# Optimization experiments

Measured on AMD Instinct MI355X. Metric: run time of the kernel, lower is better.

## Reference

```python
import jax, jax.numpy as jnp
import numpy as np

B, T, H, W, C = 2, 4, 128, 128, 192
HEADS = 6
WS = 8          # attention window (per-frame, wsD=1)
OW = 12         # overlapping KV window: 8 + int(8*0.5)
PAD = (OW - WS) // 2
TBL = (WS + OW - 1) ** 2   # 361 relative-position-bias entries
MLP_HID = C * 2


def setup_inputs() -> dict:
    key = jax.random.key(0)
    ks = jax.random.split(key, 8)
    s = 0.02
    return dict(
        x=jax.random.normal(ks[0], (B, T, H, W, C), jnp.float32),
        x_size=jnp.array([H, W], jnp.int32),  # unused by forward (shadowed), kept for signature fidelity
        rpi_oca=jax.random.randint(ks[1], (WS * WS, OW * OW), 0, TBL),
        norm1_g=jnp.ones((C,), jnp.float32), norm1_b=jnp.zeros((C,), jnp.float32),
        qkv_w=jax.random.normal(ks[2], (C, 3 * C), jnp.float32) * s,
        qkv_b=jnp.zeros((3 * C,), jnp.float32),
        rpb_table=jax.random.normal(ks[3], (TBL, HEADS), jnp.float32) * s,
        norm2_g=jnp.ones((C,), jnp.float32), norm2_b=jnp.zeros((C,), jnp.float32),
        fc1_w=jax.random.normal(ks[4], (C, MLP_HID), jnp.float32) * s,
        fc1_b=jnp.zeros((MLP_HID,), jnp.float32),
        fc2_w=jax.random.normal(ks[5], (MLP_HID, C), jnp.float32) * s,
        fc2_b=jnp.zeros((C,), jnp.float32),
    )


def _ln(x, g, b):
    m = x.mean(-1, keepdims=True)
    v = ((x - m) ** 2).mean(-1, keepdims=True)
    return (x - m) * jax.lax.rsqrt(v + 1e-5) * g + b


def reference(x, x_size, rpi_oca, norm1_g, norm1_b, qkv_w, qkv_b, rpb_table,
              norm2_g, norm2_b, fc1_w, fc1_b, fc2_w, fc2_b):
    b, t, h, w, c = x.shape
    d = c // HEADS
    scale = d ** -0.5
    nH, nW = h // WS, w // WS
    b_ = b * t * nH * nW  # total windows
    shortcut = x
    xn = _ln(x, norm1_g, norm1_b)
    qkv = (xn @ qkv_w + qkv_b).reshape(b, t, h, w, 3, c)
    q, k, v = qkv[..., 0, :], qkv[..., 1, :], qkv[..., 2, :]
    # --- query: non-overlapping (1,8,8) windows -> (b_, heads, 64, d)
    qw = (q.reshape(b, t, nH, WS, nW, WS, c)
           .transpose(0, 1, 2, 4, 3, 5, 6)
           .reshape(b_, WS * WS, HEADS, d)
           .transpose(0, 2, 1, 3))
    # --- key/value: overlapping (1,12,12) windows with stride 8, zero-padded by 2
    hid = (jnp.arange(nH) * WS)[:, None] + jnp.arange(OW)  # (nH, OW)
    wid = (jnp.arange(nW) * WS)[:, None] + jnp.arange(OW)  # (nW, OW)

    def owin(z):
        zp = jnp.pad(z, ((0, 0), (0, 0), (PAD, PAD), (PAD, PAD), (0, 0)))
        zw = zp[:, :, hid][:, :, :, :, wid]  # (b, t, nH, OW, nW, OW, c)
        return (zw.transpose(0, 1, 2, 4, 3, 5, 6)
                  .reshape(b_, OW * OW, HEADS, d)
                  .transpose(0, 2, 1, 3))

    kw, vw = owin(k), owin(v)
    attn = jnp.einsum('bhqd,bhkd->bhqk', qw * scale, kw)  # (b_, heads, 64, 144)
    bias = rpb_table[rpi_oca.reshape(-1)].reshape(WS * WS, OW * OW, HEADS).transpose(2, 0, 1)
    attn = attn + bias[None]  # NOTE: original forward applies NO softmax (self.softmax unused)
    out = (jnp.einsum('bhqk,bhkd->bhqd', attn, vw)
             .transpose(0, 2, 1, 3)
             .reshape(b_, WS * WS, c))
    # window_reverse
    xa = (out.reshape(b, t, nH, nW, WS, WS, c)
             .transpose(0, 1, 2, 4, 3, 5, 6)
             .reshape(b, t, h, w, c))
    x = xa + shortcut  # self.proj is never applied in the original forward
    hmlp = jax.nn.gelu(_ln(x, norm2_g, norm2_b) @ fc1_w + fc1_b, approximate=False)
    return x + (hmlp @ fc2_w + fc2_b)
```

## Files before the change

kernel.cpp:

```cpp
#include <hip/hip_runtime.h>
#include <cstdint>
#include <cstddef>

typedef short bf16x8 __attribute__((ext_vector_type(8)));
typedef unsigned short u16x4 __attribute__((ext_vector_type(4)));
typedef float f32x4  __attribute__((ext_vector_type(4)));
typedef unsigned short u16;

#define DEVI __device__ __forceinline__

constexpr int C     = 192;
constexpr int HEADS = 6;
constexpr int NQKV  = 576;
constexpr int HID   = 384;
constexpr int NTOK  = 131072;

DEVI u16 f2bf(float f){
  union { float f; unsigned u; } v; v.f = f;
  return (u16)((v.u + 0x7fffu + ((v.u >> 16) & 1u)) >> 16);
}

DEVI float gelu(float xx){
  float y  = xx * 0.70710678118654752f;
  float ay = fabsf(y);
  float t  = __builtin_amdgcn_rcpf(1.0f + 0.3275911f * ay);
  float p  = t*(0.254829592f + t*(-0.284496736f + t*(1.421413741f + t*(-1.453152027f + t*1.061405429f))));
  float e  = __expf(-(y*y));
  float er = copysignf(1.0f - p*e, y);
  return 0.5f * xx * (1.0f + er);
}

__global__ void prep_kernel(const float* __restrict__ qkv_w,
                            const float* __restrict__ fc1_w,
                            const float* __restrict__ fc2_w,
                            const int*   __restrict__ rpi,
                            const float* __restrict__ rpb,
                            u16* __restrict__ qkvP,
                            u16* __restrict__ fc1P,
                            u16* __restrict__ fc2P,
                            float* __restrict__ bias_pk){
  int idx = blockIdx.x * blockDim.x + threadIdx.x;
  int stride = gridDim.x * blockDim.x;
  for(int i = idx; i < 36*6*64*8; i += stride){
    int e = i & 7, lane = (i >> 3) & 63, t = i >> 9;
    int ks = t % 6, p = t / 6;
    int n = p*16 + (lane & 15), k = ks*32 + (lane >> 4)*8 + e;
    qkvP[i] = f2bf(qkv_w[k*NQKV + n]);
  }
  for(int i = idx; i < 24*6*64*8; i += stride){
    int e = i & 7, lane = (i >> 3) & 63, t = i >> 9;
    int ks = t % 6, p = t / 6;
    int n = p*16 + (lane & 15), k = ks*32 + (lane >> 4)*8 + e;
    fc1P[i] = f2bf(fc1_w[k*HID + n]);
  }
  for(int i = idx; i < 12*12*64*8; i += stride){
    int e = i & 7, lane = (i >> 3) & 63, t = i >> 9;
    int ks = t % 12, p = t / 12;
    int n = p*16 + (lane & 15), k = ks*32 + (lane >> 4)*8 + e;
    fc2P[i] = f2bf(fc2_w[k*C + n]);
  }
  const int n4 = HEADS*5*2*4*64*4;
  for(int i = idx; i < n4; i += stride){
    int t = i;
    int r    = t & 3;  t >>= 2;
    int lane = t & 63; t >>= 6;
    int mi   = t & 3;  t >>= 2;
    int nf   = t & 1;  t >>= 1;
    int chunk = t % 5; int head = t / 5;
    int q  = mi*16 + (lane & 15);
    int kk = chunk*32 + nf*16 + ((lane >> 4) << 2) + r;
    float v = 0.f;
    if(kk < 144) v = rpb[rpi[q*144 + kk]*HEADS + head];
    bias_pk[i] = v;
  }
}

__global__ __launch_bounds__(384, 4)
void qkv_kernel(const float* __restrict__ x,
                const float* __restrict__ g1,
                const float* __restrict__ b1,
                const u16* __restrict__ wP,
                const float* __restrict__ qb,
                u16* __restrict__ qkv){
  __shared__ u16 xn[64][200];
  __shared__ u16 rp[64][152];
  const int tid = threadIdx.x;
  const int bid = blockIdx.x;
  const int nh = (bid >> 3) & 1;
  const int tb = (bid & 7) + ((bid >> 4) << 3);
  const size_t tok0 = (size_t)tb * 64;
  if(tid < 256){
    const int trow = tid >> 2;
    const int j = tid & 3;
    const float* xr = x + (tok0 + trow)*C;
    float4 xv[12];
    #pragma unroll
    for(int u = 0; u < 12; ++u)
      xv[u] = *reinterpret_cast<const float4*>(xr + u*16 + j*4);
    float s1 = 0.f, s2 = 0.f;
    #pragma unroll
    for(int u = 0; u < 12; ++u){
      const float* f = reinterpret_cast<const float*>(&xv[u]);
      #pragma unroll
      for(int e = 0; e < 4; ++e){ s1 += f[e]; s2 += f[e]*f[e]; }
    }
    s1 += __shfl_xor(s1, 1, 64); s2 += __shfl_xor(s2, 1, 64);
    s1 += __shfl_xor(s1, 2, 64); s2 += __shfl_xor(s2, 2, 64);
    const float mean = s1 * (1.f/192.f);
    const float rstd = rsqrtf(s2*(1.f/192.f) - mean*mean + 1e-5f);
    #pragma unroll
    for(int u = 0; u < 12; ++u){
      const float4 gv = *reinterpret_cast<const float4*>(g1 + u*16 + j*4);
      const float4 bv = *reinterpret_cast<const float4*>(b1 + u*16 + j*4);
      const float* f = reinterpret_cast<const float*>(&xv[u]);
      const float* gp = reinterpret_cast<const float*>(&gv);
      const float* bp = reinterpret_cast<const float*>(&bv);
      u16x4 pk;
      #pragma unroll
      for(int e = 0; e < 4; ++e) pk[e] = f2bf((f[e] - mean)*rstd*gp[e] + bp[e]);
      *reinterpret_cast<u16x4*>(&xn[trow][u*16 + j*4]) = pk;
    }
  }
  __syncthreads();
  const int lane = tid & 63;
  const int wn = tid >> 6;
  const int g = lane >> 4, col = lane & 15;
  const f32x4 fzero = {0.f, 0.f, 0.f, 0.f};
  f32x4 acc[4][3];
  #pragma unroll
  for(int mi = 0; mi < 4; ++mi)
    #pragma unroll
    for(int nf = 0; nf < 3; ++nf) acc[mi][nf] = fzero;
  const int p0 = nh*18 + wn*3;
  #pragma unroll
  for(int ks = 0; ks < 6; ++ks){
    bf16x8 wf[3];
    #pragma unroll
    for(int nf = 0; nf < 3; ++nf)
      wf[nf] = *reinterpret_cast<const bf16x8*>(wP + ((size_t)(((p0 + nf)*6 + ks)*64) + lane)*8);
    bf16x8 a[4];
    #pragma unroll
    for(int mi = 0; mi < 4; ++mi)
      a[mi] = *reinterpret_cast<const bf16x8*>(&xn[mi*16 + col][ks*32 + g*8]);
    #pragma unroll
    for(int nf = 0; nf < 3; ++nf)
      #pragma unroll
      for(int mi = 0; mi < 4; ++mi)
        acc[mi][nf] = __builtin_amdgcn_mfma_f32_16x16x32_bf16(a[mi], wf[nf], acc[mi][nf], 0, 0, 0);
  }
  #pragma unroll
  for(int ph = 0; ph < 2; ++ph){
    if(wn >= ph*3 && wn < ph*3 + 3){
      const int wl = wn - ph*3;
      #pragma unroll
      for(int mi = 0; mi < 4; ++mi){
        #pragma unroll
        for(int nf = 0; nf < 3; ++nf){
          const int nloc = wl*48 + nf*16 + col;
          const float bb = qb[nh*288 + ph*144 + nloc];
          #pragma unroll
          for(int r = 0; r < 4; ++r)
            rp[mi*16 + g*4 + r][nloc] = f2bf(acc[mi][nf][r] + bb);
        }
      }
    }
    __syncthreads();
    #pragma unroll
    for(int it = 0; it < 3; ++it){
      const int c = tid + it*384;
      const int tok = c / 18, cc = c - tok*18;
      const int n0 = nh*288 + ph*144 + cc*8;
      const int pl = n0 >> 5, d0 = n0 & 31;
      bf16x8 vv = *reinterpret_cast<const bf16x8*>(&rp[tok][cc*8]);
      *reinterpret_cast<bf16x8*>(qkv + ((size_t)pl*NTOK + tok0 + tok)*32 + d0) = vv;
    }
    __syncthreads();
  }
}

__global__ __launch_bounds__(256, 4)
void attn_kernel(const u16* __restrict__ qkv,
                 const float* __restrict__ bias_pk,
                 const float* __restrict__ x,
                 float* __restrict__ out){
  __shared__ u16 Kl[160][40];
  __shared__ u16 Vt[32][168];
  __shared__ u16 Pl[64][40];
  const int tid  = threadIdx.x;
  const int lane = tid & 63;
  const int w    = tid >> 6;
  const int g = lane >> 4, col = lane & 15;
  const int win = blockIdx.x, head = blockIdx.y;
  const int bt = win >> 8, wh = (win >> 4) & 15, ww = win & 15;
  const int h0 = wh*8, w0 = ww*8;
  const size_t tokbase = (size_t)bt * 16384;
  const u16* Qp = qkv + (size_t)head      *NTOK*32;
  const u16* Kp = qkv + (size_t)(6 + head)*NTOK*32;
  const u16* Vp = qkv + (size_t)(12 + head)*NTOK*32;
  const bf16x8 z8 = {0,0,0,0,0,0,0,0};

  #pragma unroll
  for(int ii = 0; ii < 3; ++ii){
    const int i = w + ii*4;
    if(i < 10){
      const int kr = i*16 + col;
      const int r12 = (kr*2731) >> 15;
      const int c12 = kr - r12*12;
      const int hh = h0 - 2 + r12;
      const int wp = w0 - 2 + c12;
      const bool valid = (kr < 144) && (hh >= 0) && (hh < 128) && (wp >= 0) && (wp < 128);
      const size_t t = valid ? (tokbase + (size_t)hh*128 + wp) : tokbase;
      bf16x8 kv_ = *reinterpret_cast<const bf16x8*>(Kp + t*32 + g*8);
      bf16x8 vv_ = *reinterpret_cast<const bf16x8*>(Vp + t*32 + g*8);
      kv_ = valid ? kv_ : z8;
      vv_ = valid ? vv_ : z8;
      *reinterpret_cast<bf16x8*>(&Kl[kr][g*8]) = kv_;
      #pragma unroll
      for(int e = 0; e < 8; ++e) Vt[g*8 + e][kr] = (u16)vv_[e];
    }
  }
  bf16x8 qf;
  {
    const int row = w*16 + col;
    const size_t t = tokbase + (size_t)(h0 + (row >> 3))*128 + (w0 + (row & 7));
    qf = *reinterpret_cast<const bf16x8*>(Qp + t*32 + g*8);
  }
  __syncthreads();

  const f32x4 fzero = {0.f, 0.f, 0.f, 0.f};
  f32x4 oacc[2];
  oacc[0] = fzero; oacc[1] = fzero;
  const float scale = 0.17677669529663689f;

  #pragma unroll
  for(int ch = 0; ch < 5; ++ch){
    float4 bv[2];
    #pragma unroll
    for(int nf = 0; nf < 2; ++nf)
      bv[nf] = *reinterpret_cast<const float4*>(
          bias_pk + (size_t)((((head*5 + ch)*2 + nf)*4 + w)*64 + lane)*4);
    bf16x8 kfr[2];
    #pragma unroll
    for(int nf = 0; nf < 2; ++nf)
      kfr[nf] = *reinterpret_cast<const bf16x8*>(&Kl[ch*32 + nf*16 + col][g*8]);
    f32x4 st[2];
    #pragma unroll
    for(int nf = 0; nf < 2; ++nf)
      st[nf] = __builtin_amdgcn_mfma_f32_16x16x32_bf16(kfr[nf], qf, fzero, 0, 0, 0);
    #pragma unroll
    for(int nf = 0; nf < 2; ++nf){
      const float* bp = reinterpret_cast<const float*>(&bv[nf]);
      const float p0 = fmaf(st[nf][0], scale, bp[0]);
      const float p1 = fmaf(st[nf][1], scale, bp[1]);
      const float p2 = fmaf(st[nf][2], scale, bp[2]);
      const float p3 = fmaf(st[nf][3], scale, bp[3]);
      uint2 pw;
      pw.x = (unsigned)f2bf(p0) | ((unsigned)f2bf(p1) << 16);
      pw.y = (unsigned)f2bf(p2) | ((unsigned)f2bf(p3) << 16);
      *reinterpret_cast<uint2*>(
          reinterpret_cast<char*>(&Pl[0][0]) + (w*16 + col)*80 + nf*32 + g*8) = pw;
    }
    bf16x8 pa = *reinterpret_cast<const bf16x8*>(
        reinterpret_cast<const char*>(&Pl[0][0]) + (w*16 + col)*80 + g*16);
    bf16x8 vfr[2];
    #pragma unroll
    for(int nf = 0; nf < 2; ++nf)
      vfr[nf] = *reinterpret_cast<const bf16x8*>(&Vt[nf*16 + col][ch*32 + g*8]);
    #pragma unroll
    for(int nf = 0; nf < 2; ++nf)
      oacc[nf] = __builtin_amdgcn_mfma_f32_16x16x32_bf16(pa, vfr[nf], oacc[nf], 0, 0, 0);
  }
  #pragma unroll
  for(int nf = 0; nf < 2; ++nf){
    #pragma unroll
    for(int r = 0; r < 4; ++r){
      const int row = w*16 + g*4 + r;
      const int hh = h0 + (row >> 3), wp = w0 + (row & 7);
      const size_t o = (tokbase + hh*128 + wp)*(size_t)C + head*32 + nf*16 + col;
      out[o] = oacc[nf][r] + x[o];
    }
  }
}

__global__ __launch_bounds__(512, 2)
void mlp_kernel(float* __restrict__ io,
                const float* __restrict__ g2,
                const float* __restrict__ b2,
                const u16* __restrict__ w1P,
                const float* __restrict__ fb1,
                const u16* __restrict__ w2P,
                const float* __restrict__ fb2){
  __shared__ u16 xn[64][200];
  __shared__ u16 hl[64][200];
  const int tid = threadIdx.x;
  const size_t tok0 = (size_t)blockIdx.x * 64;
  {
    const int trow = tid >> 3;
    const int j = tid & 7;
    const float* xr = io + (tok0 + trow)*C;
    float4 xv[6];
    #pragma unroll
    for(int u = 0; u < 6; ++u)
      xv[u] = *reinterpret_cast<const float4*>(xr + u*32 + j*4);
    float s1 = 0.f, s2 = 0.f;
    #pragma unroll
    for(int u = 0; u < 6; ++u){
      const float* f = reinterpret_cast<const float*>(&xv[u]);
      #pragma unroll
      for(int e = 0; e < 4; ++e){ s1 += f[e]; s2 += f[e]*f[e]; }
    }
    s1 += __shfl_xor(s1, 1, 64); s2 += __shfl_xor(s2, 1, 64);
    s1 += __shfl_xor(s1, 2, 64); s2 += __shfl_xor(s2, 2, 64);
    s1 += __shfl_xor(s1, 4, 64); s2 += __shfl_xor(s2, 4, 64);
    const float mean = s1 * (1.f/192.f);
    const float rstd = rsqrtf(s2*(1.f/192.f) - mean*mean + 1e-5f);
    #pragma unroll
    for(int u = 0; u < 6; ++u){
      const float4 gv = *reinterpret_cast<const float4*>(g2 + u*32 + j*4);
      const float4 bv = *reinterpret_cast<const float4*>(b2 + u*32 + j*4);
      const float* f = reinterpret_cast<const float*>(&xv[u]);
      const float* gp = reinterpret_cast<const float*>(&gv);
      const float* bp = reinterpret_cast<const float*>(&bv);
      u16x4 pk;
      #pragma unroll
      for(int e = 0; e < 4; ++e) pk[e] = f2bf((f[e] - mean)*rstd*gp[e] + bp[e]);
      *reinterpret_cast<u16x4*>(&xn[trow][u*32 + j*4]) = pk;
    }
  }
  __syncthreads();
  const int lane = tid & 63, wave = tid >> 6;
  const int wm = wave >> 2;
  const int wn = wave & 3;
  const int g = lane >> 4, col = lane & 15;
  const f32x4 fzero = {0.f, 0.f, 0.f, 0.f};
  f32x4 acc2[2][3];
  #pragma unroll
  for(int mi = 0; mi < 2; ++mi)
    #pragma unroll
    for(int nf = 0; nf < 3; ++nf) acc2[mi][nf] = fzero;
  #pragma unroll
  for(int hb = 0; hb < 2; ++hb){
    f32x4 acc1[2][3];
    #pragma unroll
    for(int mi = 0; mi < 2; ++mi)
      #pragma unroll
      for(int nf = 0; nf < 3; ++nf) acc1[mi][nf] = fzero;
    #pragma unroll
    for(int ks = 0; ks < 6; ++ks){
      bf16x8 wf[3];
      #pragma unroll
      for(int nf = 0; nf < 3; ++nf)
        wf[nf] = *reinterpret_cast<const bf16x8*>(w1P + ((size_t)(((hb*12 + wn*3 + nf)*6 + ks)*64) + lane)*8);
      bf16x8 a[2];
      #pragma unroll
      for(int mi = 0; mi < 2; ++mi)
        a[mi] = *reinterpret_cast<const bf16x8*>(&xn[wm*32 + mi*16 + col][ks*32 + g*8]);
      #pragma unroll
      for(int nf = 0; nf < 3; ++nf)
        #pragma unroll
        for(int mi = 0; mi < 2; ++mi)
          acc1[mi][nf] = __builtin_amdgcn_mfma_f32_16x16x32_bf16(a[mi], wf[nf], acc1[mi][nf], 0, 0, 0);
    }
    #pragma unroll
    for(int mi = 0; mi < 2; ++mi){
      #pragma unroll
      for(int nf = 0; nf < 3; ++nf){
        const int nl = wn*48 + nf*16 + col;
        const float bb = fb1[hb*192 + nl];
        #pragma unroll
        for(int r = 0; r < 4; ++r){
          const int row = wm*32 + mi*16 + g*4 + r;
          hl[row][nl] = f2bf(gelu(acc1[mi][nf][r] + bb));
        }
      }
    }
    __syncthreads();
    #pragma unroll
    for(int ks = 0; ks < 6; ++ks){
      bf16x8 wf[3];
      #pragma unroll
      for(int nf = 0; nf < 3; ++nf)
        wf[nf] = *reinterpret_cast<const bf16x8*>(w2P + ((size_t)(((wn*3 + nf)*12 + hb*6 + ks)*64) + lane)*8);
      bf16x8 a[2];
      #pragma unroll
      for(int mi = 0; mi < 2; ++mi)
        a[mi] = *reinterpret_cast<const bf16x8*>(&hl[wm*32 + mi*16 + col][ks*32 + g*8]);
      #pragma unroll
      for(int nf = 0; nf < 3; ++nf)
        #pragma unroll
        for(int mi = 0; mi < 2; ++mi)
          acc2[mi][nf] = __builtin_amdgcn_mfma_f32_16x16x32_bf16(a[mi], wf[nf], acc2[mi][nf], 0, 0, 0);
    }
    __syncthreads();
  }
  #pragma unroll
  for(int mi = 0; mi < 2; ++mi){
    #pragma unroll
    for(int nf = 0; nf < 3; ++nf){
      const int n = wn*48 + nf*16 + col;
      const float bb = fb2[n];
      #pragma unroll
      for(int r = 0; r < 4; ++r){
        const int row = wm*32 + mi*16 + g*4 + r;
        const size_t idx = (tok0 + row)*C + n;
        io[idx] = acc2[mi][nf][r] + bb + io[idx];
      }
    }
  }
}

extern "C" void kernel_launch(void* const* d_in, const int* in_sizes, int n_in,
                              void* d_out, int out_size, void* d_ws, size_t ws_size,
                              hipStream_t stream){
  const float* x    = (const float*)d_in[0];
  const int*   rpi  = (const int*)  d_in[2];
  const float* n1g  = (const float*)d_in[3];
  const float* n1b  = (const float*)d_in[4];
  const float* qkvw = (const float*)d_in[5];
  const float* qkvb = (const float*)d_in[6];
  const float* rpb  = (const float*)d_in[7];
  const float* n2g  = (const float*)d_in[8];
  const float* n2b  = (const float*)d_in[9];
  const float* fc1w = (const float*)d_in[10];
  const float* fc1b = (const float*)d_in[11];
  const float* fc2w = (const float*)d_in[12];
  const float* fc2b = (const float*)d_in[13];
  float* out = (float*)d_out;
  char* ws = (char*)d_ws;
  u16*   qkvP    = (u16*)  (ws + 0);
  u16*   fc1P    = (u16*)  (ws + 221184);
  u16*   fc2P    = (u16*)  (ws + 368640);
  float* bias_pk = (float*)(ws + 516096);
  u16*   qkvbuf  = (u16*)  (ws + 1499136);
  if(ws_size < 152494080ull) return;
  prep_kernel<<<dim3(512), dim3(256), 0, stream>>>(qkvw, fc1w, fc2w, rpi, rpb, qkvP, fc1P, fc2P, bias_pk);
  qkv_kernel<<<dim3(4096), dim3(384), 0, stream>>>(x, n1g, n1b, qkvP, qkvb, qkvbuf);
  attn_kernel<<<dim3(2048, 6), dim3(256), 0, stream>>>(qkvbuf, bias_pk, x, out);
  mlp_kernel<<<dim3(2048), dim3(512), 0, stream>>>(out, n2g, n2b, fc1P, fc1b, fc2P, fc2b);
}
```

Before: 281.9 us.

## Coalesce attention and MLP epilogues through LDS, shrink MLP hidden tile for occupancy

The attention kernel now stages its output tile in shared memory, which aliases the K/V buffers, and writes the residual-added result as float4 vectors instead of scattered scalar stores. The MLP kernel splits the hidden dimension into three 128-wide chunks to shrink the hidden-activation buffer and raises the launch-bounds occupancy targets. Its fc2 output is staged through LDS for a vectorized residual add. Risks: the MLP output is rounded to bf16 before the residual add, which loses precision, and the higher occupancy targets may cause register spills.

```diff
diff --git a/kernel.cpp b/kernel.cpp
--- a/kernel.cpp
+++ b/kernel.cpp
@@ -18,6 +18,10 @@
 DEVI u16 f2bf(float f){
   union { float f; unsigned u; } v; v.f = f;
   return (u16)((v.u + 0x7fffu + ((v.u >> 16) & 1u)) >> 16);
+}
+DEVI float bf2f(u16 h){
+  union { unsigned u; float f; } v; v.u = ((unsigned)h) << 16;
+  return v.f;
 }
 
 DEVI float gelu(float xx){
@@ -178,14 +182,16 @@
   }
 }
 
-__global__ __launch_bounds__(256, 4)
+__global__ __launch_bounds__(256, 5)
 void attn_kernel(const u16* __restrict__ qkv,
                  const float* __restrict__ bias_pk,
                  const float* __restrict__ x,
                  float* __restrict__ out){
-  __shared__ u16 Kl[160][40];
-  __shared__ u16 Vt[32][168];
-  __shared__ u16 Pl[64][40];
+  __shared__ alignas(16) char smem[28672];
+  u16 (*Kl)[40]  = reinterpret_cast<u16(*)[40]>(smem);
+  u16 (*Vt)[168] = reinterpret_cast<u16(*)[168]>(smem + 12800);
+  char* Plb      = smem + 23552;
+  float (*Of)[36] = reinterpret_cast<float(*)[36]>(smem);
   const int tid  = threadIdx.x;
   const int lane = tid & 63;
   const int w    = tid >> 6;
@@ -257,11 +263,9 @@
       uint2 pw;
       pw.x = (unsigned)f2bf(p0) | ((unsigned)f2bf(p1) << 16);
       pw.y = (unsigned)f2bf(p2) | ((unsigned)f2bf(p3) << 16);
-      *reinterpret_cast<uint2*>(
-          reinterpret_cast<char*>(&Pl[0][0]) + (w*16 + col)*80 + nf*32 + g*8) = pw;
-    }
-    bf16x8 pa = *reinterpret_cast<const bf16x8*>(
-        reinterpret_cast<const char*>(&Pl[0][0]) + (w*16 + col)*80 + g*16);
+      *reinterpret_cast<uint2*>(Plb + (w*16 + col)*80 + nf*32 + g*8) = pw;
+    }
+    bf16x8 pa = *reinterpret_cast<const bf16x8*>(Plb + (w*16 + col)*80 + g*16);
     bf16x8 vfr[2];
     #pragma unroll
     for(int nf = 0; nf < 2; ++nf)
@@ -270,19 +274,29 @@
     for(int nf = 0; nf < 2; ++nf)
       oacc[nf] = __builtin_amdgcn_mfma_f32_16x16x32_bf16(pa, vfr[nf], oacc[nf], 0, 0, 0);
   }
-  #pragma unroll
-  for(int nf = 0; nf < 2; ++nf){
-    #pragma unroll
-    for(int r = 0; r < 4; ++r){
-      const int row = w*16 + g*4 + r;
-      const int hh = h0 + (row >> 3), wp = w0 + (row & 7);
-      const size_t o = (tokbase + hh*128 + wp)*(size_t)C + head*32 + nf*16 + col;
-      out[o] = oacc[nf][r] + x[o];
-    }
-  }
-}
-
-__global__ __launch_bounds__(512, 2)
+  __syncthreads();
+  #pragma unroll
+  for(int nf = 0; nf < 2; ++nf)
+    #pragma unroll
+    for(int r = 0; r < 4; ++r)
+      Of[w*16 + g*4 + r][nf*16 + col] = oacc[nf][r];
+  __syncthreads();
+  {
+    const int tok = tid >> 2, q = tid & 3;
+    const int hh = h0 + (tok >> 3), wp = w0 + (tok & 7);
+    const size_t o = (tokbase + (size_t)hh*128 + wp)*(size_t)C + head*32 + q*8;
+    float4 a0 = *reinterpret_cast<const float4*>(&Of[tok][q*8]);
+    float4 a1 = *reinterpret_cast<const float4*>(&Of[tok][q*8 + 4]);
+    const float4 x0 = *reinterpret_cast<const float4*>(x + o);
+    const float4 x1 = *reinterpret_cast<const float4*>(x + o + 4);
+    a0.x += x0.x; a0.y += x0.y; a0.z += x0.z; a0.w += x0.w;
+    a1.x += x1.x; a1.y += x1.y; a1.z += x1.z; a1.w += x1.w;
+    *reinterpret_cast<float4*>(out + o)     = a0;
+    *reinterpret_cast<float4*>(out + o + 4) = a1;
+  }
+}
+
+__global__ __launch_bounds__(512, 6)
 void mlp_kernel(float* __restrict__ io,
                 const float* __restrict__ g2,
                 const float* __restrict__ b2,
@@ -291,7 +305,7 @@
                 const u16* __restrict__ w2P,
                 const float* __restrict__ fb2){
   __shared__ u16 xn[64][200];
-  __shared__ u16 hl[64][200];
+  __shared__ u16 hq[64][136];
   const int tid = threadIdx.x;
   const size_t tok0 = (size_t)blockIdx.x * 64;
   {
@@ -339,24 +353,24 @@
     #pragma unroll
     for(int nf = 0; nf < 3; ++nf) acc2[mi][nf] = fzero;
   #pragma unroll
-  for(int hb = 0; hb < 2; ++hb){
-    f32x4 acc1[2][3];
-    #pragma unroll
-    for(int mi = 0; mi < 2; ++mi)
-      #pragma unroll
-      for(int nf = 0; nf < 3; ++nf) acc1[mi][nf] = fzero;
+  for(int hb = 0; hb < 3; ++hb){
+    f32x4 acc1[2][2];
+    #pragma unroll
+    for(int mi = 0; mi < 2; ++mi){ acc1[mi][0] = fzero; acc1[mi][1] = fzero; }
     #pragma unroll
     for(int ks = 0; ks < 6; ++ks){
-      bf16x8 wf[3];
-      #pragma unroll
-      for(int nf = 0; nf < 3; ++nf)
-        wf[nf] = *reinterpret_cast<const bf16x8*>(w1P + ((size_t)(((hb*12 + wn*3 + nf)*6 + ks)*64) + lane)*8);
+      bf16x8 wf[2];
+      #pragma unroll
+      for(int nf = 0; nf < 2; ++nf){
+        const int p = hb*8 + wn*2 + nf;
+        wf[nf] = *reinterpret_cast<const bf16x8*>(w1P + ((size_t)((p*6 + ks)*64) + lane)*8);
+      }
       bf16x8 a[2];
       #pragma unroll
       for(int mi = 0; mi < 2; ++mi)
         a[mi] = *reinterpret_cast<const bf16x8*>(&xn[wm*32 + mi*16 + col][ks*32 + g*8]);
       #pragma unroll
-      for(int nf = 0; nf < 3; ++nf)
+      for(int nf = 0; nf < 2; ++nf)
         #pragma unroll
         for(int mi = 0; mi < 2; ++mi)
           acc1[mi][nf] = __builtin_amdgcn_mfma_f32_16x16x32_bf16(a[mi], wf[nf], acc1[mi][nf], 0, 0, 0);
@@ -364,27 +378,28 @@
     #pragma unroll
     for(int mi = 0; mi < 2; ++mi){
       #pragma unroll
-      for(int nf = 0; nf < 3; ++nf){
-        const int nl = wn*48 + nf*16 + col;
-        const float bb = fb1[hb*192 + nl];
+      for(int nf = 0; nf < 2; ++nf){
+        const int nl = wn*32 + nf*16 + col;
+        const float bb = fb1[hb*128 + nl];
         #pragma unroll
         for(int r = 0; r < 4; ++r){
           const int row = wm*32 + mi*16 + g*4 + r;
-          hl[row][nl] = f2bf(gelu(acc1[mi][nf][r] + bb));
+          hq[row][nl] = f2bf(gelu(acc1[mi][nf][r] + bb));
         }
       }
     }
     __syncthreads();
     #pragma unroll
-    for(int ks = 0; ks < 6; ++ks){
+    for(int ks = 0; ks < 4; ++ks){
+      const int ksg = hb*4 + ks;
       bf16x8 wf[3];
       #pragma unroll
       for(int nf = 0; nf < 3; ++nf)
-        wf[nf] = *reinterpret_cast<const bf16x8*>(w2P + ((size_t)(((wn*3 + nf)*12 + hb*6 + ks)*64) + lane)*8);
+        wf[nf] = *reinterpret_cast<const bf16x8*>(w2P + ((size_t)(((wn*3 + nf)*12 + ksg)*64) + lane)*8);
       bf16x8 a[2];
       #pragma unroll
       for(int mi = 0; mi < 2; ++mi)
-        a[mi] = *reinterpret_cast<const bf16x8*>(&hl[wm*32 + mi*16 + col][ks*32 + g*8]);
+        a[mi] = *reinterpret_cast<const bf16x8*>(&hq[wm*32 + mi*16 + col][ks*32 + g*8]);
       #pragma unroll
       for(int nf = 0; nf < 3; ++nf)
         #pragma unroll
@@ -402,9 +417,20 @@
       #pragma unroll
       for(int r = 0; r < 4; ++r){
         const int row = wm*32 + mi*16 + g*4 + r;
-        const size_t idx = (tok0 + row)*C + n;
-        io[idx] = acc2[mi][nf][r] + bb + io[idx];
+        xn[row][n] = f2bf(acc2[mi][nf][r] + bb);
       }
+    }
+  }
+  __syncthreads();
+  {
+    const int trow = tid >> 3, j = tid & 7;
+    float* xr = io + (tok0 + trow)*C + j*24;
+    #pragma unroll
+    for(int u = 0; u < 6; ++u){
+      const u16x4 s = *reinterpret_cast<const u16x4*>(&xn[trow][j*24 + u*4]);
+      float4 v = *reinterpret_cast<const float4*>(xr + u*4);
+      v.x += bf2f(s[0]); v.y += bf2f(s[1]); v.z += bf2f(s[2]); v.w += bf2f(s[3]);
+      *reinterpret_cast<float4*>(xr + u*4) = v;
     }
   }
 }
```

Result: slower. 313.4 us (+11.2%).
